# Optimization experiments

Measured on AMD Instinct MI355X. Metric: run time of the kernel, lower is better.

Reference implementation:

```python
import jax, jax.numpy as jnp
import numpy as np

IN_DIM, OUT_DIM = 96, 32
D = IN_DIM + OUT_DIM  # 128, feature dim of x
H, KQ = 8, 64         # head_num, KQ_dim
GAMMA = 1e-4


def setup_inputs() -> dict:
    key = jax.random.key(0)
    kx, kk, kq, kv = jax.random.split(key, 4)
    B, N = 32, 2048
    std_kq = (GAMMA / D) ** 0.5
    return {
        "x": jax.random.normal(kx, (B, N, D), dtype=jnp.float32),
        # nn.Linear weight shape [out_features, in_features]; stacked per head
        "Wk": jax.random.normal(kk, (H, KQ, D), dtype=jnp.float32) * std_kq,
        "Wq": jax.random.normal(kq, (H, KQ, D), dtype=jnp.float32) * std_kq,
        "Wv": jax.random.normal(kv, (H, D, D), dtype=jnp.float32) * GAMMA,
    }


def reference(x, Wk, Wq, Wv):
    # Per-head projections (nn.Linear: y = x @ W^T), stacked over heads h
    K = jnp.einsum("bnd,hkd->bhnk", x, Wk)  # [B,H,N,KQ]
    Q = jnp.einsum("bnd,hkd->bhnk", x, Wq)  # [B,H,N,KQ]
    V = jnp.einsum("bnd,hed->bhne", x, Wv)  # [B,H,N,D]
    # No softmax -> (Q K^T) V == Q (K^T V); use the O(n d^2) associative form
    KtV = jnp.einsum("bhnk,bhne->bhke", K, V)  # [B,H,KQ,D]
    # sum over heads folded into the contraction
    out = jnp.einsum("bhnk,bhke->bne", Q, KtV)  # [B,N,D]
    return out
```

## Files before the change

kernel.cpp:

```cpp
#include <hip/hip_runtime.h>

#define BB 32
#define NN 2048
#define DD 128
#define HH 8
#define KK 64

typedef __attribute__((ext_vector_type(8))) short bf16x8;
typedef __attribute__((ext_vector_type(4))) float f32x4;
#define MFMA_BF16 __builtin_amdgcn_mfma_f32_16x16x32_bf16


__device__ __forceinline__ float bf2f(unsigned short h){ return __uint_as_float(((unsigned)h) << 16); }
__device__ __forceinline__ unsigned short f2bf(float f){
  unsigned u = __float_as_uint(f);
  u += 0x7fffu + ((u >> 16) & 1u);
  return (unsigned short)(u >> 16);
}

__device__ __forceinline__ bf16x8 ldfrag_sw(const unsigned short* base, int row16, int kc, int lane){
  int d = row16 + (lane & 15);
  int q = lane >> 4;
  int ch = ((kc << 2) + q) ^ (d & 7);
  return *(const bf16x8*)(base + d*128 + ch*8);
}
__device__ __forceinline__ bf16x8 ldfrag_pad(const unsigned short* base, int row16, int kc, int lane){
  int r = row16 + (lane & 15);
  int q = lane >> 4;
  return *(const bf16x8*)(base + r*136 + kc*32 + q*8);
}

__global__ __launch_bounds__(512, 4) void kgkp(const float* __restrict__ x,
                                               const float* __restrict__ Wq,
                                               const float* __restrict__ Wk,
                                               unsigned short* __restrict__ Gp_bf,
                                               unsigned short* __restrict__ Pbf){
  __shared__ __align__(16) unsigned short sm[32768];
  const int t = threadIdx.x;
  const int bid = blockIdx.x;
  const int w = t >> 6, lane = t & 63, quad = lane >> 4;
  if (bid < 512){
    unsigned short* xh = sm;
    unsigned short* xl = sm + 16384;
    const int b = bid & 31, chunk = bid >> 5;
    const float* xb = x + ((size_t)b*NN + (size_t)chunk*128)*DD;
    for (int it = 0; it < 2; ++it){
      int gidx = it*512 + t;
      int n4g = (gidx & 7) | (((gidx >> 6) & 3) << 3);
      int dcq = ((gidx >> 3) & 7) | (((gidx >> 8) & 3) << 3);
      float4 v[4];
      #pragma unroll
      for (int j = 0; j < 4; ++j)
        v[j] = *(const float4*)(xb + (size_t)(n4g*4 + j)*DD + dcq*4);
      #pragma unroll
      for (int i = 0; i < 4; ++i){
        int d = dcq*4 + i;
        float f0 = (&v[0].x)[i], f1 = (&v[1].x)[i], f2 = (&v[2].x)[i], f3 = (&v[3].x)[i];
        unsigned short h0 = f2bf(f0), h1 = f2bf(f1), h2 = f2bf(f2), h3 = f2bf(f3);
        unsigned short l0 = f2bf(f0 - bf2f(h0)), l1 = f2bf(f1 - bf2f(h1));
        unsigned short l2 = f2bf(f2 - bf2f(h2)), l3 = f2bf(f3 - bf2f(h3));
        int off = d*128 + ((((n4g >> 1) ^ (d & 7)) << 3) + (n4g & 1)*4);
        *(ushort4*)(xh + off) = make_ushort4(h0, h1, h2, h3);
        *(ushort4*)(xl + off) = make_ushort4(l0, l1, l2, l3);
      }
    }
    __syncthreads();
    const int wr = (w >> 1)*32, wc = (w & 1)*64;
    f32x4 acc[2][4] = {};
    for (int kc = 0; kc < 4; ++kc){
      bf16x8 ah[2], al[2], bh[4], bl[4];
      #pragma unroll
      for (int r = 0; r < 2; ++r){
        ah[r] = ldfrag_sw(xh, wr + r*16, kc, lane);
        al[r] = ldfrag_sw(xl, wr + r*16, kc, lane);
      }
      #pragma unroll
      for (int c = 0; c < 4; ++c){
        bh[c] = ldfrag_sw(xh, wc + c*16, kc, lane);
        bl[c] = ldfrag_sw(xl, wc + c*16, kc, lane);
      }
      #pragma unroll
      for (int r = 0; r < 2; ++r)
        #pragma unroll
        for (int c = 0; c < 4; ++c){
          acc[r][c] = MFMA_BF16(ah[r], bh[c], acc[r][c], 0, 0, 0);
          acc[r][c] = MFMA_BF16(ah[r], bl[c], acc[r][c], 0, 0, 0);
          acc[r][c] = MFMA_BF16(al[r], bh[c], acc[r][c], 0, 0, 0);
        }
    }
    __syncthreads();
    float* Sf = (float*)sm;
    #pragma unroll
    for (int r = 0; r < 2; ++r)
      #pragma unroll
      for (int c = 0; c < 4; ++c)
        #pragma unroll
        for (int reg = 0; reg < 4; ++reg)
          Sf[(wr + r*16 + quad*4 + reg)*128 + wc + c*16 + (lane & 15)] = acc[r][c][reg];
    __syncthreads();
    unsigned short* gp = Gp_bf + ((size_t)(chunk*32 + b) << 14);
    for (int i = t; i < 2048; i += 512){
      int r = i >> 4, c8 = (i & 15) * 8;
      const float* s = Sf + r*128 + c8;
      *(ushort4*)(gp + r*128 + c8)     = make_ushort4(f2bf(s[0]), f2bf(s[1]), f2bf(s[2]), f2bf(s[3]));
      *(ushort4*)(gp + r*128 + c8 + 4) = make_ushort4(f2bf(s[4]), f2bf(s[5]), f2bf(s[6]), f2bf(s[7]));
    }
  } else {
    float* Aq = (float*)sm;
    float* Bk = Aq + 64*36;
    const int kpid = bid - 512;
    const int h = kpid >> 2, rt = kpid & 3;
    const int i0 = rt * 32;
    const int tr = t >> 6, tc = t & 63;
    const float* wq = Wq + h*KK*DD;
    const float* wk = Wk + h*KK*DD;
    for (int i = t; i < 512; i += 512){
      int k = i >> 3, c4 = (i & 7) << 2;
      *(float4*)(&Aq[k*36 + c4]) = *(const float4*)(wq + k*DD + i0 + c4);
    }
    for (int i = t; i < 2048; i += 512){
      int k = i >> 5, c4 = (i & 31) << 2;
      *(float4*)(&Bk[k*132 + c4]) = *(const float4*)(wk + k*DD + c4);
    }
    __syncthreads();
    float acc[4][2] = {};
    for (int k = 0; k < 64; k += 2){
      float a0[4], a1[4], b0[2], b1[2];
      *(float4*)a0 = *(float4*)(&Aq[k*36 + tr*4]);
      *(float4*)a1 = *(float4*)(&Aq[(k+1)*36 + tr*4]);
      b0[0] = Bk[k*132 + tc*2];     b0[1] = Bk[k*132 + tc*2 + 1];
      b1[0] = Bk[(k+1)*132 + tc*2]; b1[1] = Bk[(k+1)*132 + tc*2 + 1];
      #pragma unroll
      for (int i = 0; i < 4; ++i)
        #pragma unroll
        for (int j = 0; j < 2; ++j){
          acc[i][j] += a0[i]*b0[j];
          acc[i][j] += a1[i]*b1[j];
        }
    }
    unsigned short* Ph = Pbf + h*DD*DD;
    #pragma unroll
    for (int i = 0; i < 4; ++i)
      *(ushort2*)(&Ph[(i0 + tr*4 + i)*DD + tc*2]) =
          make_ushort2(f2bf(acc[i][0]), f2bf(acc[i][1]));
  }
}

__global__ __launch_bounds__(512, 4) void km2(const unsigned short* __restrict__ Gp_bf,
                                              const float* __restrict__ Wv,
                                              const unsigned short* __restrict__ Pbf,
                                              unsigned short* __restrict__ Mpt_bf){
  __shared__ __align__(16) unsigned short As[128*136];
  __shared__ __align__(16) unsigned short Bs[64*136];
  const int bid = blockIdx.x;
  const int b = bid & 31, h = (bid >> 5) & 7, eh = bid >> 8;
  const int e0 = eh * 64;
  const int t = threadIdx.x;
  const int w = t >> 6, lane = t & 63, quad = lane >> 4;
  for (int i = t; i < 2048; i += 512){
    int r = i >> 4, c8 = (i & 15) * 8;
    float s[8] = {};
    #pragma unroll
    for (int p = 0; p < 16; ++p){
      uint4 u = *(const uint4*)(Gp_bf + (((size_t)(p*32 + b)) << 14) + r*128 + c8);
      const unsigned short* pu = (const unsigned short*)&u;
      #pragma unroll
      for (int j = 0; j < 8; ++j) s[j] += bf2f(pu[j]);
    }
    *(ushort4*)(As + r*136 + c8)     = make_ushort4(f2bf(s[0]), f2bf(s[1]), f2bf(s[2]), f2bf(s[3]));
    *(ushort4*)(As + r*136 + c8 + 4) = make_ushort4(f2bf(s[4]), f2bf(s[5]), f2bf(s[6]), f2bf(s[7]));
  }
  const float* Wvh = Wv + ((size_t)h*DD + e0)*DD;
  for (int i = t; i < 2048; i += 512){
    int e = i >> 5, dc = (i & 31) * 4;
    float4 v = *(const float4*)(Wvh + (size_t)e*DD + dc);
    *(ushort4*)(Bs + e*136 + dc) = make_ushort4(f2bf(v.x), f2bf(v.y), f2bf(v.z), f2bf(v.w));
  }
  __syncthreads();
  const int wr = (w >> 1)*32, wc = (w & 1)*32;
  f32x4 acc1[2][2] = {};
  for (int kc = 0; kc < 4; ++kc){
    bf16x8 a[2], bb[2];
    #pragma unroll
    for (int r = 0; r < 2; ++r) a[r] = ldfrag_pad(As, wr + r*16, kc, lane);
    #pragma unroll
    for (int c = 0; c < 2; ++c) bb[c] = ldfrag_pad(Bs, wc + c*16, kc, lane);
    #pragma unroll
    for (int r = 0; r < 2; ++r)
      #pragma unroll
      for (int c = 0; c < 2; ++c)
        acc1[r][c] = MFMA_BF16(a[r], bb[c], acc1[r][c], 0, 0, 0);
  }
  __syncthreads();
  #pragma unroll
  for (int r = 0; r < 2; ++r)
    #pragma unroll
    for (int c = 0; c < 2; ++c){
      int e = wc + c*16 + (lane & 15);
      int c0 = wr + r*16 + quad*4;
      *(ushort4*)(Bs + e*136 + c0) = make_ushort4(f2bf(acc1[r][c][0]), f2bf(acc1[r][c][1]),
                                                  f2bf(acc1[r][c][2]), f2bf(acc1[r][c][3]));
    }
  const unsigned short* Ph = Pbf + h*DD*DD;
  for (int i = t; i < 2048; i += 512){
    int r = i >> 4, ch = (i & 15) * 8;
    *(uint4*)(As + r*136 + ch) = *(const uint4*)(Ph + r*128 + ch);
  }
  __syncthreads();
  f32x4 acc2[2][2] = {};
  for (int kc = 0; kc < 4; ++kc){
    bf16x8 a[2], bb[2];
    #pragma unroll
    for (int r = 0; r < 2; ++r) a[r] = ldfrag_pad(As, wr + r*16, kc, lane);
    #pragma unroll
    for (int c = 0; c < 2; ++c) bb[c] = ldfrag_pad(Bs, wc + c*16, kc, lane);
    #pragma unroll
    for (int r = 0; r < 2; ++r)
      #pragma unroll
      for (int c = 0; c < 2; ++c)
        acc2[r][c] = MFMA_BF16(a[r], bb[c], acc2[r][c], 0, 0, 0);
  }
  __syncthreads();
  float* Af = (float*)As;
  #pragma unroll
  for (int r = 0; r < 2; ++r)
    #pragma unroll
    for (int c = 0; c < 2; ++c){
      int e = wc + c*16 + (lane & 15);
      int d0 = wr + r*16 + quad*4;
      *(float4*)(Af + e*132 + d0) = make_float4(acc2[r][c][0], acc2[r][c][1], acc2[r][c][2], acc2[r][c][3]);
    }
  __syncthreads();
  unsigned short* Mb = Mpt_bf + (((size_t)(b*8 + h)) << 14);
  for (int i = t; i < 1024; i += 512){
    int e = i >> 4, c8 = (i & 15) * 8;
    const float* s = Af + e*132 + c8;
    *(ushort4*)(Mb + (e0 + e)*128 + c8)     = make_ushort4(f2bf(s[0]), f2bf(s[1]), f2bf(s[2]), f2bf(s[3]));
    *(ushort4*)(Mb + (e0 + e)*128 + c8 + 4) = make_ushort4(f2bf(s[4]), f2bf(s[5]), f2bf(s[6]), f2bf(s[7]));
  }
}

__global__ __launch_bounds__(512, 4) void ko2(const float* __restrict__ x,
                                              const unsigned short* __restrict__ Mpt_bf,
                                              float* __restrict__ out){
  __shared__ __align__(16) unsigned short sm[32768];
  unsigned short* xs = sm;
  unsigned short* Ms = sm + 16384;
  const int bid = blockIdx.x;
  const int b = bid & 31, nt = bid >> 5;
  const int t = threadIdx.x;
  const int w = t >> 6, lane = t & 63, quad = lane >> 4;
  const float* xb = x + ((size_t)b*NN + (size_t)nt*128)*DD;
  for (int i = t; i < 4096; i += 512){
    int n = i >> 5, dcq = i & 31;
    float4 v = *(const float4*)(xb + (size_t)n*DD + dcq*4);
    int off = n*128 + ((((dcq >> 1) ^ (n & 7)) << 3) + (dcq & 1)*4);
    *(ushort4*)(xs + off) = make_ushort4(f2bf(v.x), f2bf(v.y), f2bf(v.z), f2bf(v.w));
  }
  for (int i = t; i < 2048; i += 512){
    int e = i >> 4, c8 = (i & 15) * 8;
    float s[8] = {};
    #pragma unroll
    for (int h = 0; h < 8; ++h){
      uint4 u = *(const uint4*)(Mpt_bf + (((size_t)(b*8 + h)) << 14) + e*128 + c8);
      const unsigned short* pu = (const unsigned short*)&u;
      #pragma unroll
      for (int j = 0; j < 8; ++j) s[j] += bf2f(pu[j]);
    }
    int off = e*128 + (((c8 >> 3) ^ (e & 7)) << 3);
    *(ushort4*)(Ms + off)     = make_ushort4(f2bf(s[0]), f2bf(s[1]), f2bf(s[2]), f2bf(s[3]));
    *(ushort4*)(Ms + off + 4) = make_ushort4(f2bf(s[4]), f2bf(s[5]), f2bf(s[6]), f2bf(s[7]));
  }
  __syncthreads();
  const int wr = (w >> 1)*32, wc = (w & 1)*64;
  f32x4 acc[2][4] = {};
  for (int kc = 0; kc < 4; ++kc){
    bf16x8 a[2], bb[4];
    #pragma unroll
    for (int r = 0; r < 2; ++r) a[r] = ldfrag_sw(xs, wr + r*16, kc, lane);
    #pragma unroll
    for (int c = 0; c < 4; ++c) bb[c] = ldfrag_sw(Ms, wc + c*16, kc, lane);
    #pragma unroll
    for (int r = 0; r < 2; ++r)
      #pragma unroll
      for (int c = 0; c < 4; ++c)
        acc[r][c] = MFMA_BF16(a[r], bb[c], acc[r][c], 0, 0, 0);
  }
  __syncthreads();
  float* Sf = (float*)sm;
  #pragma unroll
  for (int r = 0; r < 2; ++r)
    #pragma unroll
    for (int c = 0; c < 4; ++c)
      #pragma unroll
      for (int reg = 0; reg < 4; ++reg)
        Sf[(wr + r*16 + quad*4 + reg)*128 + wc + c*16 + (lane & 15)] = acc[r][c][reg];
  __syncthreads();
  float* ob = out + ((size_t)b*NN + (size_t)nt*128)*DD;
  for (int i = t; i < 4096; i += 512){
    int n = i >> 5, c4 = (i & 31) * 4;
    *(float4*)(ob + (size_t)n*DD + c4) = *(const float4*)(Sf + n*128 + c4);
  }
}

extern "C" void kernel_launch(void* const* d_in, const int* in_sizes, int n_in,
                              void* d_out, int out_size, void* d_ws, size_t ws_size,
                              hipStream_t stream){
  const float* x  = (const float*)d_in[0];
  const float* Wk = (const float*)d_in[1];
  const float* Wq = (const float*)d_in[2];
  const float* Wv = (const float*)d_in[3];
  float* out = (float*)d_out;
  float* ws = (float*)d_ws;
  unsigned short* Gp_bf  = (unsigned short*)ws;
  unsigned short* Mpt_bf = (unsigned short*)(ws + 4194304);
  unsigned short* Pbf    = (unsigned short*)(ws + 6291456);

  kgkp<<<544, 512, 0, stream>>>(x, Wq, Wk, Gp_bf, Pbf);
  km2 <<<512, 512, 0, stream>>>(Gp_bf, Wv, Pbf, Mpt_bf);
  ko2 <<<512, 512, 0, stream>>>(x, Mpt_bf, out);
}
```

Baseline: 128.9 us.

## Rebalance Gram partials, widen km2 tiles, add head-reduction kernel

The Gram-matrix kernel now has each block accumulate two 128-row chunks, which halves the number of bf16 partials written and later reduced. km2 computes the full 128-wide e tile per (b,h) with swizzled LDS instead of splitting into two halves. A new kmr kernel reduces the per-head M matrices once per batch, so ko2 only copies a single reduced M instead of summing 8 heads in every one of its 16 n-tile blocks. Stores are packed into 128-bit writes. The cost is an extra kernel launch and fewer blocks with more serial work per block in kgkp and km2.

```diff
diff --git a/kernel.cpp b/kernel.cpp
--- a/kernel.cpp
+++ b/kernel.cpp
@@ -17,17 +17,15 @@
   u += 0x7fffu + ((u >> 16) & 1u);
   return (unsigned short)(u >> 16);
 }
+__device__ __forceinline__ unsigned pack2(float a, float b){
+  return (unsigned)f2bf(a) | ((unsigned)f2bf(b) << 16);
+}
 
 __device__ __forceinline__ bf16x8 ldfrag_sw(const unsigned short* base, int row16, int kc, int lane){
   int d = row16 + (lane & 15);
   int q = lane >> 4;
   int ch = ((kc << 2) + q) ^ (d & 7);
   return *(const bf16x8*)(base + d*128 + ch*8);
-}
-__device__ __forceinline__ bf16x8 ldfrag_pad(const unsigned short* base, int row16, int kc, int lane){
-  int r = row16 + (lane & 15);
-  int q = lane >> 4;
-  return *(const bf16x8*)(base + r*136 + kc*32 + q*8);
 }
 
 __global__ __launch_bounds__(512, 4) void kgkp(const float* __restrict__ x,
@@ -39,54 +37,57 @@
   const int t = threadIdx.x;
   const int bid = blockIdx.x;
   const int w = t >> 6, lane = t & 63, quad = lane >> 4;
-  if (bid < 512){
+  if (bid < 256){
     unsigned short* xh = sm;
     unsigned short* xl = sm + 16384;
     const int b = bid & 31, chunk = bid >> 5;
-    const float* xb = x + ((size_t)b*NN + (size_t)chunk*128)*DD;
-    for (int it = 0; it < 2; ++it){
-      int gidx = it*512 + t;
-      int n4g = (gidx & 7) | (((gidx >> 6) & 3) << 3);
-      int dcq = ((gidx >> 3) & 7) | (((gidx >> 8) & 3) << 3);
-      float4 v[4];
-      #pragma unroll
-      for (int j = 0; j < 4; ++j)
-        v[j] = *(const float4*)(xb + (size_t)(n4g*4 + j)*DD + dcq*4);
-      #pragma unroll
-      for (int i = 0; i < 4; ++i){
-        int d = dcq*4 + i;
-        float f0 = (&v[0].x)[i], f1 = (&v[1].x)[i], f2 = (&v[2].x)[i], f3 = (&v[3].x)[i];
-        unsigned short h0 = f2bf(f0), h1 = f2bf(f1), h2 = f2bf(f2), h3 = f2bf(f3);
-        unsigned short l0 = f2bf(f0 - bf2f(h0)), l1 = f2bf(f1 - bf2f(h1));
-        unsigned short l2 = f2bf(f2 - bf2f(h2)), l3 = f2bf(f3 - bf2f(h3));
-        int off = d*128 + ((((n4g >> 1) ^ (d & 7)) << 3) + (n4g & 1)*4);
-        *(ushort4*)(xh + off) = make_ushort4(h0, h1, h2, h3);
-        *(ushort4*)(xl + off) = make_ushort4(l0, l1, l2, l3);
-      }
-    }
-    __syncthreads();
     const int wr = (w >> 1)*32, wc = (w & 1)*64;
     f32x4 acc[2][4] = {};
-    for (int kc = 0; kc < 4; ++kc){
-      bf16x8 ah[2], al[2], bh[4], bl[4];
-      #pragma unroll
-      for (int r = 0; r < 2; ++r){
-        ah[r] = ldfrag_sw(xh, wr + r*16, kc, lane);
-        al[r] = ldfrag_sw(xl, wr + r*16, kc, lane);
+    for (int sub = 0; sub < 2; ++sub){
+      if (sub) __syncthreads();
+      const float* xb = x + ((size_t)b*NN + (size_t)(chunk*256 + sub*128))*DD;
+      for (int it = 0; it < 2; ++it){
+        int gidx = it*512 + t;
+        int n4g = (gidx & 7) | (((gidx >> 6) & 3) << 3);
+        int dcq = ((gidx >> 3) & 7) | (((gidx >> 8) & 3) << 3);
+        float4 v[4];
+        #pragma unroll
+        for (int j = 0; j < 4; ++j)
+          v[j] = *(const float4*)(xb + (size_t)(n4g*4 + j)*DD + dcq*4);
+        #pragma unroll
+        for (int i = 0; i < 4; ++i){
+          int d = dcq*4 + i;
+          float f0 = (&v[0].x)[i], f1 = (&v[1].x)[i], f2 = (&v[2].x)[i], f3 = (&v[3].x)[i];
+          unsigned short h0 = f2bf(f0), h1 = f2bf(f1), h2 = f2bf(f2), h3 = f2bf(f3);
+          unsigned short l0 = f2bf(f0 - bf2f(h0)), l1 = f2bf(f1 - bf2f(h1));
+          unsigned short l2 = f2bf(f2 - bf2f(h2)), l3 = f2bf(f3 - bf2f(h3));
+          int off = d*128 + ((((n4g >> 1) ^ (d & 7)) << 3) + (n4g & 1)*4);
+          *(ushort4*)(xh + off) = make_ushort4(h0, h1, h2, h3);
+          *(ushort4*)(xl + off) = make_ushort4(l0, l1, l2, l3);
+        }
       }
-      #pragma unroll
-      for (int c = 0; c < 4; ++c){
-        bh[c] = ldfrag_sw(xh, wc + c*16, kc, lane);
-        bl[c] = ldfrag_sw(xl, wc + c*16, kc, lane);
+      __syncthreads();
+      for (int kc = 0; kc < 4; ++kc){
+        bf16x8 ah[2], al[2], bh[4], bl[4];
+        #pragma unroll
+        for (int r = 0; r < 2; ++r){
+          ah[r] = ldfrag_sw(xh, wr + r*16, kc, lane);
+          al[r] = ldfrag_sw(xl, wr + r*16, kc, lane);
+        }
+        #pragma unroll
+        for (int c = 0; c < 4; ++c){
+          bh[c] = ldfrag_sw(xh, wc + c*16, kc, lane);
+          bl[c] = ldfrag_sw(xl, wc + c*16, kc, lane);
+        }
+        #pragma unroll
+        for (int r = 0; r < 2; ++r)
+          #pragma unroll
+          for (int c = 0; c < 4; ++c){
+            acc[r][c] = MFMA_BF16(ah[r], bh[c], acc[r][c], 0, 0, 0);
+            acc[r][c] = MFMA_BF16(ah[r], bl[c], acc[r][c], 0, 0, 0);
+            acc[r][c] = MFMA_BF16(al[r], bh[c], acc[r][c], 0, 0, 0);
+          }
       }
-      #pragma unroll
-      for (int r = 0; r < 2; ++r)
-        #pragma unroll
-        for (int c = 0; c < 4; ++c){
-          acc[r][c] = MFMA_BF16(ah[r], bh[c], acc[r][c], 0, 0, 0);
-          acc[r][c] = MFMA_BF16(ah[r], bl[c], acc[r][c], 0, 0, 0);
-          acc[r][c] = MFMA_BF16(al[r], bh[c], acc[r][c], 0, 0, 0);
-        }
     }
     __syncthreads();
     float* Sf = (float*)sm;
@@ -102,13 +103,15 @@
     for (int i = t; i < 2048; i += 512){
       int r = i >> 4, c8 = (i & 15) * 8;
       const float* s = Sf + r*128 + c8;
-      *(ushort4*)(gp + r*128 + c8)     = make_ushort4(f2bf(s[0]), f2bf(s[1]), f2bf(s[2]), f2bf(s[3]));
-      *(ushort4*)(gp + r*128 + c8 + 4) = make_ushort4(f2bf(s[4]), f2bf(s[5]), f2bf(s[6]), f2bf(s[7]));
+      uint4 o;
+      o.x = pack2(s[0], s[1]); o.y = pack2(s[2], s[3]);
+      o.z = pack2(s[4], s[5]); o.w = pack2(s[6], s[7]);
+      *(uint4*)(gp + r*128 + c8) = o;
     }
   } else {
     float* Aq = (float*)sm;
     float* Bk = Aq + 64*36;
-    const int kpid = bid - 512;
+    const int kpid = bid - 256;
     const int h = kpid >> 2, rt = kpid & 3;
     const int i0 = rt * 32;
     const int tr = t >> 6, tc = t & 63;
@@ -146,102 +149,121 @@
   }
 }
 
-__global__ __launch_bounds__(512, 4) void km2(const unsigned short* __restrict__ Gp_bf,
+__global__ __launch_bounds__(512, 2) void km2(const unsigned short* __restrict__ Gp_bf,
                                               const float* __restrict__ Wv,
                                               const unsigned short* __restrict__ Pbf,
-                                              unsigned short* __restrict__ Mpt_bf){
-  __shared__ __align__(16) unsigned short As[128*136];
-  __shared__ __align__(16) unsigned short Bs[64*136];
+                                              unsigned short* __restrict__ Mp_bf){
+  __shared__ __align__(16) unsigned short sm[32768];
+  unsigned short* As = sm;
+  unsigned short* Bs = sm + 16384;
   const int bid = blockIdx.x;
-  const int b = bid & 31, h = (bid >> 5) & 7, eh = bid >> 8;
-  const int e0 = eh * 64;
+  const int b = bid & 31, h = bid >> 5;
   const int t = threadIdx.x;
   const int w = t >> 6, lane = t & 63, quad = lane >> 4;
   for (int i = t; i < 2048; i += 512){
     int r = i >> 4, c8 = (i & 15) * 8;
     float s[8] = {};
     #pragma unroll
-    for (int p = 0; p < 16; ++p){
+    for (int p = 0; p < 8; ++p){
       uint4 u = *(const uint4*)(Gp_bf + (((size_t)(p*32 + b)) << 14) + r*128 + c8);
       const unsigned short* pu = (const unsigned short*)&u;
       #pragma unroll
       for (int j = 0; j < 8; ++j) s[j] += bf2f(pu[j]);
     }
-    *(ushort4*)(As + r*136 + c8)     = make_ushort4(f2bf(s[0]), f2bf(s[1]), f2bf(s[2]), f2bf(s[3]));
-    *(ushort4*)(As + r*136 + c8 + 4) = make_ushort4(f2bf(s[4]), f2bf(s[5]), f2bf(s[6]), f2bf(s[7]));
-  }
-  const float* Wvh = Wv + ((size_t)h*DD + e0)*DD;
-  for (int i = t; i < 2048; i += 512){
+    uint4 o;
+    o.x = pack2(s[0], s[1]); o.y = pack2(s[2], s[3]);
+    o.z = pack2(s[4], s[5]); o.w = pack2(s[6], s[7]);
+    *(uint4*)(As + r*128 + ((((c8 >> 3) ^ (r & 7))) << 3)) = o;
+  }
+  const float* Wvh = Wv + (size_t)h*DD*DD;
+  for (int i = t; i < 4096; i += 512){
     int e = i >> 5, dc = (i & 31) * 4;
     float4 v = *(const float4*)(Wvh + (size_t)e*DD + dc);
-    *(ushort4*)(Bs + e*136 + dc) = make_ushort4(f2bf(v.x), f2bf(v.y), f2bf(v.z), f2bf(v.w));
-  }
-  __syncthreads();
-  const int wr = (w >> 1)*32, wc = (w & 1)*32;
-  f32x4 acc1[2][2] = {};
+    int off = e*128 + ((((dc >> 3) ^ (e & 7)) << 3) + (dc & 4));
+    *(ushort4*)(Bs + off) = make_ushort4(f2bf(v.x), f2bf(v.y), f2bf(v.z), f2bf(v.w));
+  }
+  __syncthreads();
+  f32x4 acc1[8] = {};
   for (int kc = 0; kc < 4; ++kc){
-    bf16x8 a[2], bb[2];
-    #pragma unroll
-    for (int r = 0; r < 2; ++r) a[r] = ldfrag_pad(As, wr + r*16, kc, lane);
-    #pragma unroll
-    for (int c = 0; c < 2; ++c) bb[c] = ldfrag_pad(Bs, wc + c*16, kc, lane);
-    #pragma unroll
-    for (int r = 0; r < 2; ++r)
-      #pragma unroll
-      for (int c = 0; c < 2; ++c)
-        acc1[r][c] = MFMA_BF16(a[r], bb[c], acc1[r][c], 0, 0, 0);
+    bf16x8 a = ldfrag_sw(As, w*16, kc, lane);
+    bf16x8 bb[8];
+    #pragma unroll
+    for (int c = 0; c < 8; ++c) bb[c] = ldfrag_sw(Bs, c*16, kc, lane);
+    #pragma unroll
+    for (int c = 0; c < 8; ++c) acc1[c] = MFMA_BF16(a, bb[c], acc1[c], 0, 0, 0);
   }
   __syncthreads();
   #pragma unroll
-  for (int r = 0; r < 2; ++r)
-    #pragma unroll
-    for (int c = 0; c < 2; ++c){
-      int e = wc + c*16 + (lane & 15);
-      int c0 = wr + r*16 + quad*4;
-      *(ushort4*)(Bs + e*136 + c0) = make_ushort4(f2bf(acc1[r][c][0]), f2bf(acc1[r][c][1]),
-                                                  f2bf(acc1[r][c][2]), f2bf(acc1[r][c][3]));
-    }
-  const unsigned short* Ph = Pbf + h*DD*DD;
+  for (int c = 0; c < 8; ++c){
+    int e = c*16 + (lane & 15);
+    int d0 = w*16 + quad*4;
+    int off = e*128 + ((((d0 >> 3) ^ (e & 7)) << 3) + (d0 & 7));
+    *(ushort4*)(Bs + off) = make_ushort4(f2bf(acc1[c][0]), f2bf(acc1[c][1]),
+                                         f2bf(acc1[c][2]), f2bf(acc1[c][3]));
+  }
+  const unsigned short* Ph = Pbf + (size_t)h*DD*DD;
   for (int i = t; i < 2048; i += 512){
-    int r = i >> 4, ch = (i & 15) * 8;
-    *(uint4*)(As + r*136 + ch) = *(const uint4*)(Ph + r*128 + ch);
-  }
-  __syncthreads();
-  f32x4 acc2[2][2] = {};
+    int r = i >> 4, ch = i & 15;
+    *(uint4*)(As + r*128 + ((ch ^ (r & 7)) << 3)) = *(const uint4*)(Ph + r*128 + ch*8);
+  }
+  __syncthreads();
+  f32x4 acc2[8] = {};
   for (int kc = 0; kc < 4; ++kc){
-    bf16x8 a[2], bb[2];
-    #pragma unroll
-    for (int r = 0; r < 2; ++r) a[r] = ldfrag_pad(As, wr + r*16, kc, lane);
-    #pragma unroll
-    for (int c = 0; c < 2; ++c) bb[c] = ldfrag_pad(Bs, wc + c*16, kc, lane);
-    #pragma unroll
-    for (int r = 0; r < 2; ++r)
-      #pragma unroll
-      for (int c = 0; c < 2; ++c)
-        acc2[r][c] = MFMA_BF16(a[r], bb[c], acc2[r][c], 0, 0, 0);
-  }
-  __syncthreads();
-  float* Af = (float*)As;
+    bf16x8 a = ldfrag_sw(As, w*16, kc, lane);
+    bf16x8 bb[8];
+    #pragma unroll
+    for (int c = 0; c < 8; ++c) bb[c] = ldfrag_sw(Bs, c*16, kc, lane);
+    #pragma unroll
+    for (int c = 0; c < 8; ++c) acc2[c] = MFMA_BF16(a, bb[c], acc2[c], 0, 0, 0);
+  }
+  __syncthreads();
+  float* Sf = (float*)sm;
   #pragma unroll
-  for (int r = 0; r < 2; ++r)
-    #pragma unroll
-    for (int c = 0; c < 2; ++c){
-      int e = wc + c*16 + (lane & 15);
-      int d0 = wr + r*16 + quad*4;
-      *(float4*)(Af + e*132 + d0) = make_float4(acc2[r][c][0], acc2[r][c][1], acc2[r][c][2], acc2[r][c][3]);
-    }
-  __syncthreads();
-  unsigned short* Mb = Mpt_bf + (((size_t)(b*8 + h)) << 14);
-  for (int i = t; i < 1024; i += 512){
-    int e = i >> 4, c8 = (i & 15) * 8;
-    const float* s = Af + e*132 + c8;
-    *(ushort4*)(Mb + (e0 + e)*128 + c8)     = make_ushort4(f2bf(s[0]), f2bf(s[1]), f2bf(s[2]), f2bf(s[3]));
-    *(ushort4*)(Mb + (e0 + e)*128 + c8 + 4) = make_ushort4(f2bf(s[4]), f2bf(s[5]), f2bf(s[6]), f2bf(s[7]));
+  for (int c = 0; c < 8; ++c)
+    #pragma unroll
+    for (int reg = 0; reg < 4; ++reg)
+      Sf[(w*16 + quad*4 + reg)*128 + c*16 + (lane & 15)] = acc2[c][reg];
+  __syncthreads();
+  unsigned short* Mb = Mp_bf + (((size_t)(b*8 + h)) << 14);
+  for (int i = t; i < 2048; i += 512){
+    int r = i >> 4, c8 = (i & 15) * 8;
+    const float* s = Sf + r*128 + c8;
+    uint4 o;
+    o.x = pack2(s[0], s[1]); o.y = pack2(s[2], s[3]);
+    o.z = pack2(s[4], s[5]); o.w = pack2(s[6], s[7]);
+    *(uint4*)(Mb + r*128 + c8) = o;
+  }
+}
+
+__global__ __launch_bounds__(256) void kmr(const unsigned short* __restrict__ Mp_bf,
+                                           unsigned short* __restrict__ Mtbf){
+  __shared__ float Sf[16][132];
+  const int bid = blockIdx.x;
+  const int b = bid >> 3, es = bid & 7;
+  const int t = threadIdx.x;
+  {
+    int d = t >> 1, half = t & 1;
+    float s[8] = {};
+    #pragma unroll
+    for (int h = 0; h < 8; ++h){
+      uint4 u = *(const uint4*)(Mp_bf + (((size_t)(b*8 + h)) << 14) + d*128 + es*16 + half*8);
+      const unsigned short* pu = (const unsigned short*)&u;
+      #pragma unroll
+      for (int j = 0; j < 8; ++j) s[j] += bf2f(pu[j]);
+    }
+    #pragma unroll
+    for (int j = 0; j < 8; ++j) Sf[half*8 + j][d] = s[j];
+  }
+  __syncthreads();
+  unsigned short* Mb = Mtbf + ((size_t)b << 14);
+  for (int j = t; j < 2048; j += 256){
+    int e = j >> 7, d = j & 127;
+    Mb[(es*16 + e)*128 + d] = f2bf(Sf[e][d]);
   }
 }
 
 __global__ __launch_bounds__(512, 4) void ko2(const float* __restrict__ x,
-                                              const unsigned short* __restrict__ Mpt_bf,
+                                              const unsigned short* __restrict__ Mtbf,
                                               float* __restrict__ out){
   __shared__ __align__(16) unsigned short sm[32768];
   unsigned short* xs = sm;
@@ -251,6 +273,7 @@
   const int t = threadIdx.x;
   const int w = t >> 6, lane = t & 63, quad = lane >> 4;
   const float* xb = x + ((size_t)b*NN + (size_t)nt*128)*DD;
+  const unsigned short* Mtb = Mtbf + ((size_t)b << 14);
   for (int i = t; i < 4096; i += 512){
     int n = i >> 5, dcq = i & 31;
     float4 v = *(const float4*)(xb + (size_t)n*DD + dcq*4);
@@ -258,18 +281,8 @@
     *(ushort4*)(xs + off) = make_ushort4(f2bf(v.x), f2bf(v.y), f2bf(v.z), f2bf(v.w));
   }
   for (int i = t; i < 2048; i += 512){
-    int e = i >> 4, c8 = (i & 15) * 8;
-    float s[8] = {};
-    #pragma unroll
-    for (int h = 0; h < 8; ++h){
-      uint4 u = *(const uint4*)(Mpt_bf + (((size_t)(b*8 + h)) << 14) + e*128 + c8);
-      const unsigned short* pu = (const unsigned short*)&u;
-      #pragma unroll
-      for (int j = 0; j < 8; ++j) s[j] += bf2f(pu[j]);
-    }
-    int off = e*128 + (((c8 >> 3) ^ (e & 7)) << 3);
-    *(ushort4*)(Ms + off)     = make_ushort4(f2bf(s[0]), f2bf(s[1]), f2bf(s[2]), f2bf(s[3]));
-    *(ushort4*)(Ms + off + 4) = make_ushort4(f2bf(s[4]), f2bf(s[5]), f2bf(s[6]), f2bf(s[7]));
+    int e = i >> 4, ng = i & 15;
+    *(uint4*)(Ms + e*128 + ((ng ^ (e & 7)) << 3)) = *(const uint4*)(Mtb + e*128 + ng*8);
   }
   __syncthreads();
   const int wr = (w >> 1)*32, wc = (w & 1)*64;
@@ -311,12 +324,14 @@
   const float* Wq = (const float*)d_in[2];
   const float* Wv = (const float*)d_in[3];
   float* out = (float*)d_out;
-  float* ws = (float*)d_ws;
-  unsigned short* Gp_bf  = (unsigned short*)ws;
-  unsigned short* Mpt_bf = (unsigned short*)(ws + 4194304);
-  unsigned short* Pbf    = (unsigned short*)(ws + 6291456);
-
-  kgkp<<<544, 512, 0, stream>>>(x, Wq, Wk, Gp_bf, Pbf);
-  km2 <<<512, 512, 0, stream>>>(Gp_bf, Wv, Pbf, Mpt_bf);
-  ko2 <<<512, 512, 0, stream>>>(x, Mpt_bf, out);
-}
+  unsigned short* wsu = (unsigned short*)d_ws;
+  unsigned short* Gp_bf = wsu;
+  unsigned short* Mp_bf = wsu + 4194304;
+  unsigned short* Pbf   = wsu + 8388608;
+  unsigned short* Mtbf  = wsu + 8519680;
+
+  kgkp<<<288, 512, 0, stream>>>(x, Wq, Wk, Gp_bf, Pbf);
+  km2 <<<256, 512, 0, stream>>>(Gp_bf, Wv, Pbf, Mp_bf);
+  kmr <<<256, 256, 0, stream>>>(Mp_bf, Mtbf);
+  ko2 <<<512, 512, 0, stream>>>(x, Mtbf, out);
+}
```

Result: faster. 123.5 us (-4.2%).
